# Kernel optimization log

Measured on AMD Instinct MI355X. Metric: run time of the kernel, lower is better.

Reference implementation:

```python
import jax, jax.numpy as jnp
import numpy as np

B, S, D, E, L = 8, 512, 768, 768, 4000

def setup_inputs() -> dict:
    key = jax.random.key(0)
    k1, k2, k3, k4 = jax.random.split(key, 4)
    last_hidden_state = jax.random.normal(k1, (B, S, D), dtype=jnp.float32)
    label_feat = jax.random.normal(k2, (L, E), dtype=jnp.float32)
    # nn.Linear(D, E): weight [E, D], bias [E]; xavier-ish scale
    W = jax.random.normal(k3, (E, D), dtype=jnp.float32) * (1.0 / np.sqrt(D))
    bias = jax.random.normal(k4, (E,), dtype=jnp.float32) * 0.01
    return {"last_hidden_state": last_hidden_state, "label_feat": label_feat, "W": W, "bias": bias}

def reference(last_hidden_state, label_feat, W, bias):
    # proj: tanh(Linear(last_hidden_state))  -> [B, S, E]
    proj = jnp.tanh(jnp.einsum('bsd,ed->bse', last_hidden_state, W) + bias)
    # scores: bmm(label_feat [B,L,E], proj^T [B,E,S]) -> [B, L, S]
    scores = jnp.einsum('le,bse->bls', label_feat, proj)
    # softmax over dim=1 (the LABEL dim), as in the original
    weights = jax.nn.softmax(scores, axis=1)
    # attn: bmm(weights [B,L,S], last_hidden_state [B,S,D]) -> [B, L, D]
    attn_output = jnp.einsum('bls,bsd->bld', weights, last_hidden_state)
    return (weights, attn_output)
```

## Files before the change

### kernel.cpp

```cpp
#include <hip/hip_runtime.h>
#include <hip/hip_bf16.h>
#include <cmath>

typedef __attribute__((ext_vector_type(8))) short short8;
typedef __attribute__((ext_vector_type(4))) float f32x4;

#define SM_CH 16
#define WCH   32

__device__ inline ushort f2bf(float x) {
    union { float f; unsigned u; } v; v.f = x;
    unsigned r = v.u + 0x7FFF + ((v.u >> 16) & 1);
    return (ushort)(r >> 16);
}

__device__ inline void split2(float x, ushort& hi, ushort& lo) {
    union { float f; unsigned u; } v; v.f = x;
    hi = (ushort)(v.u >> 16);
    union { float f; unsigned u; } h; h.u = v.u & 0xFFFF0000u;
    union { float f; unsigned u; } d; d.f = x - h.f;
    lo = (ushort)(d.u >> 16);
}

__device__ inline int swz(int row, int byte_in_row) {
    return row * 128 + (byte_in_row ^ ((row & 7) << 4));
}

__device__ inline void gload16(const void* g, void* lds) {
    __builtin_amdgcn_global_load_lds(
        (const __attribute__((address_space(1))) unsigned int*)g,
        (__attribute__((address_space(3))) unsigned int*)lds, 16, 0, 0);
}

__device__ inline void xcd_remap(int& bx, int& by, int& bz) {
    unsigned nx = gridDim.x, ny = gridDim.y;
    unsigned nwg = nx * ny * gridDim.z;
    unsigned id = blockIdx.x + nx * (blockIdx.y + ny * blockIdx.z);
    unsigned q = nwg >> 3;
    unsigned s = (id & 7) * q + (id >> 3);
    bx = s % nx; unsigned r = s / nx;
    by = r % ny; bz = r / ny;
}

__global__ __launch_bounds__(512, 2) void mfma_sc2(
    const ushort* __restrict__ AH, const ushort* __restrict__ AL,
    const ushort* __restrict__ BH, const ushort* __restrict__ BL,
    float* __restrict__ Cb, float* __restrict__ pmo, float* __restrict__ pso,
    int M, int N, long long sB, long long sC)
{
    extern __shared__ char smem[];
    const int K = 768;

    int bx, by, bz; xcd_remap(bx, by, bz);
    const int bm = bx * 256;
    const int bn = by * 256;
    const long long z = bz;

    const ushort* BHb = BH + z * sB;
    const ushort* BLb = BL + z * sB;

    const int t    = threadIdx.x;
    const int lane = t & 63;
    const int w    = t >> 6;
    const int wr   = w >> 2;
    const int wc   = w & 3;
    const int lrow = lane & 15;
    const int kg16 = (lane >> 4) * 16;

    const ushort* srcA[4]; const ushort* srcB[4]; int ldsO[4];
    #pragma unroll
    for (int i = 0; i < 4; ++i) {
        const int row  = w * 32 + i * 8 + (lane >> 3);
        const int q    = (lane & 7) ^ (row & 7);
        const int colo = (q & 3) * 8;
        srcA[i] = ((q < 4) ? AH : AL) + (long long)min(bm + row, M - 1) * K + colo;
        srcB[i] = ((q < 4) ? BHb : BLb) + (long long)(bn + row) * K + colo;
        ldsO[i] = w * 4096 + i * 1024;
    }

#define STAGE(k0_, cur_)                                                      \
    {                                                                         \
        _Pragma("unroll")                                                     \
        for (int i = 0; i < 4; ++i) {                                         \
            gload16(srcA[i] + (k0_), smem + (cur_) * 32768 + ldsO[i]);        \
            gload16(srcB[i] + (k0_), smem + 65536 + (cur_) * 32768 + ldsO[i]);\
        }                                                                     \
    }

    STAGE(0, 0);
    STAGE(32, 1);
    asm volatile("s_waitcnt vmcnt(8)" ::: "memory");
    __builtin_amdgcn_s_barrier();

    f32x4 acc[8][4] = {};

    for (int tt = 0; tt < 24; ++tt) {
        const int cur = tt & 1;
        const char* Ab = smem + cur * 32768;
        const char* Bb = smem + 65536 + cur * 32768;

        __builtin_amdgcn_s_setprio(1);
        short8 bh[4], bl[4];
        #pragma unroll
        for (int n = 0; n < 4; ++n) {
            bh[n] = *(const short8*)(Bb + swz(wc * 64 + n * 16 + lrow, kg16));
            bl[n] = *(const short8*)(Bb + swz(wc * 64 + n * 16 + lrow, 64 + kg16));
        }
        #pragma unroll
        for (int g = 0; g < 2; ++g) {
            short8 ah[4], al[4];
            #pragma unroll
            for (int m4 = 0; m4 < 4; ++m4) {
                const int r = wr * 128 + (g * 4 + m4) * 16 + lrow;
                ah[m4] = *(const short8*)(Ab + swz(r, kg16));
                al[m4] = *(const short8*)(Ab + swz(r, 64 + kg16));
            }
            #pragma unroll
            for (int m4 = 0; m4 < 4; ++m4)
                #pragma unroll
                for (int n = 0; n < 4; ++n) {
                    acc[g*4+m4][n] = __builtin_amdgcn_mfma_f32_16x16x32_bf16(
                        al[m4], bh[n], acc[g*4+m4][n], 0, 0, 0);
                    acc[g*4+m4][n] = __builtin_amdgcn_mfma_f32_16x16x32_bf16(
                        ah[m4], bl[n], acc[g*4+m4][n], 0, 0, 0);
                    acc[g*4+m4][n] = __builtin_amdgcn_mfma_f32_16x16x32_bf16(
                        ah[m4], bh[n], acc[g*4+m4][n], 0, 0, 0);
                }
        }
        __builtin_amdgcn_s_setprio(0);

        asm volatile("s_waitcnt lgkmcnt(0)" ::: "memory");
        __builtin_amdgcn_s_barrier();

        if (tt + 2 < 24) {
            STAGE((tt + 2) * 32, cur);
            asm volatile("s_waitcnt vmcnt(8)" ::: "memory");
        } else {
            asm volatile("s_waitcnt vmcnt(0)" ::: "memory");
        }
        __builtin_amdgcn_s_barrier();
    }
#undef STAGE

    float* C = Cb + z * sC;
    const int r0 = bm + wr * 128 + (lane >> 4) * 4;
    const int c0 = bn + wc * 64 + (lane & 15);
    #pragma unroll
    for (int n = 0; n < 4; ++n) {
        const int col = c0 + n * 16;
        #pragma unroll
        for (int mi = 0; mi < 8; ++mi) {
            #pragma unroll
            for (int r = 0; r < 4; ++r) {
                const int row = r0 + mi * 16 + r;
                if (row < M) C[(long long)row * N + col] = acc[mi][n][r];
            }
        }
    }

    __syncthreads();
    float* red = (float*)smem;
    const int slot = wr * 4 + (lane >> 4);
    const int colb = wc * 64 + (lane & 15);

    float lm[4];
    #pragma unroll
    for (int n = 0; n < 4; ++n) {
        float v = -INFINITY;
        #pragma unroll
        for (int mi = 0; mi < 8; ++mi)
            #pragma unroll
            for (int r = 0; r < 4; ++r)
                if (r0 + mi * 16 + r < M) v = fmaxf(v, acc[mi][n][r]);
        lm[n] = v;
    }
    #pragma unroll
    for (int n = 0; n < 4; ++n)
        red[(colb + n * 16) * 8 + slot] = lm[n];
    __syncthreads();
    float cm[4];
    #pragma unroll
    for (int n = 0; n < 4; ++n) {
        float v = -INFINITY;
        #pragma unroll
        for (int s8 = 0; s8 < 8; ++s8)
            v = fmaxf(v, red[(colb + n * 16) * 8 + s8]);
        cm[n] = v;
    }
    __syncthreads();
    float ls[4];
    #pragma unroll
    for (int n = 0; n < 4; ++n) {
        float sum = 0.f;
        #pragma unroll
        for (int mi = 0; mi < 8; ++mi)
            #pragma unroll
            for (int r = 0; r < 4; ++r)
                if (r0 + mi * 16 + r < M) sum += __expf(acc[mi][n][r] - cm[n]);
        ls[n] = sum;
    }
    #pragma unroll
    for (int n = 0; n < 4; ++n)
        red[(colb + n * 16) * 8 + slot] = ls[n];
    __syncthreads();
    if (slot == 0) {
        #pragma unroll
        for (int n = 0; n < 4; ++n) {
            float sum = 0.f;
            #pragma unroll
            for (int s8 = 0; s8 < 8; ++s8)
                sum += red[(colb + n * 16) * 8 + s8];
            const int col = bn + colb + n * 16;
            pmo[(z * SM_CH + bx) * N + col] = cm[n];
            pso[(z * SM_CH + bx) * N + col] = sum;
        }
    }
}

template<int ROWS, int KS>
__device__ inline void stage_plane(const ushort* __restrict__ src,
                                   char* plane, int t, int rbase, int rmax)
{
    #pragma unroll
    for (int s = 0; s < ROWS / 64; ++s) {
        const int row = s * 64 + (t >> 3);
        const int col = (((t & 7) * 16) ^ ((row & 7) << 4)) >> 1;
        const int gr  = min(rbase + row, rmax);
        gload16(src + (long long)gr * KS + col,
                plane + s * 8192 + (t >> 6) * 1024);
    }
}

__global__ __launch_bounds__(512, 2) void mfma_attn8(
    const ushort* __restrict__ A, const ushort* __restrict__ B,
    float* __restrict__ Cb, int M, int N,
    long long sA, long long sB, long long sC)
{
    extern __shared__ char smem[];
    constexpr int ABYTES = 128 * 128;
    constexpr int NT = 8, KS = 512;

    int bx, by, bz; xcd_remap(bx, by, bz);
    const int bm = bx * 128;
    const int bn = by * 256;
    const long long z = bz;

    const ushort* Ab_g = A + z * sA;
    const ushort* Bb_g = B + z * sB;

    const int t    = threadIdx.x;
    const int lane = t & 63;
    const int w    = t >> 6;
    const int wr   = w >> 2;
    const int wc   = w & 3;
    const int lrow = lane & 15;
    const int kg16 = (lane >> 4) * 16;

    stage_plane<128, KS>(Ab_g, smem, t, bm, M - 1);
    stage_plane<256, KS>(Bb_g, smem + 2 * ABYTES, t, bn, N - 1);
    stage_plane<128, KS>(Ab_g + 64, smem + ABYTES, t, bm, M - 1);
    stage_plane<256, KS>(Bb_g + 64, smem + 2 * ABYTES + 32768, t, bn, N - 1);
    asm volatile("s_waitcnt vmcnt(6)" ::: "memory");
    __builtin_amdgcn_s_barrier();

    f32x4 acc[4][4] = {};

    for (int tt = 0; tt < NT; ++tt) {
        const int cur = tt & 1;
        char* Ab = smem + cur * ABYTES;
        char* Bb = smem + 2 * ABYTES + cur * 32768;

        __builtin_amdgcn_s_setprio(1);
        short8 bf[4][2];
        #pragma unroll
        for (int n = 0; n < 4; ++n)
            #pragma unroll
            for (int ks = 0; ks < 2; ++ks)
                bf[n][ks] = *(const short8*)(Bb + swz(wc * 64 + n * 16 + lrow,
                                                      ks * 64 + kg16));
        #pragma unroll
        for (int q = 0; q < 2; ++q) {
            short8 af[2][2];
            #pragma unroll
            for (int mi = 0; mi < 2; ++mi)
                #pragma unroll
                for (int ks = 0; ks < 2; ++ks)
                    af[mi][ks] = *(const short8*)(Ab +
                        swz(wr * 64 + (q * 2 + mi) * 16 + lrow, ks * 64 + kg16));
            #pragma unroll
            for (int ks = 0; ks < 2; ++ks)
                #pragma unroll
                for (int mi = 0; mi < 2; ++mi)
                    #pragma unroll
                    for (int n = 0; n < 4; ++n)
                        acc[q * 2 + mi][n] = __builtin_amdgcn_mfma_f32_16x16x32_bf16(
                            af[mi][ks], bf[n][ks], acc[q * 2 + mi][n], 0, 0, 0);
        }
        __builtin_amdgcn_s_setprio(0);

        asm volatile("s_waitcnt lgkmcnt(0)" ::: "memory");
        __builtin_amdgcn_s_barrier();

        if (tt + 2 < NT) {
            stage_plane<128, KS>(Ab_g + (tt + 2) * 64, smem + cur * ABYTES,
                                 t, bm, M - 1);
            stage_plane<256, KS>(Bb_g + (tt + 2) * 64,
                                 smem + 2 * ABYTES + cur * 32768, t, bn, N - 1);
            asm volatile("s_waitcnt vmcnt(6)" ::: "memory");
        } else {
            asm volatile("s_waitcnt vmcnt(0)" ::: "memory");
        }
        __builtin_amdgcn_s_barrier();
    }

    float* C = Cb + z * sC;
    const int r0 = bm + wr * 64 + (lane >> 4) * 4;
    const int c0 = bn + wc * 64 + (lane & 15);
    #pragma unroll
    for (int n = 0; n < 4; ++n) {
        const int col = c0 + n * 16;
        #pragma unroll
        for (int mi = 0; mi < 4; ++mi) {
            #pragma unroll
            for (int r = 0; r < 4; ++r) {
                const int row = r0 + mi * 16 + r;
                if (row < M) C[(long long)row * N + col] = acc[mi][n][r];
            }
        }
    }
}

__global__ __launch_bounds__(256) void split_planes_kernel(
    const float* __restrict__ in, ushort* __restrict__ H,
    ushort* __restrict__ L, long long n4)
{
    long long i = (long long)blockIdx.x * 256 + threadIdx.x;
    if (i >= n4) return;
    float4 v = *(const float4*)(in + i * 4);
    ushort h[4], l[4];
    split2(v.x, h[0], l[0]); split2(v.y, h[1], l[1]);
    split2(v.z, h[2], l[2]); split2(v.w, h[3], l[3]);
    *(ushort4*)(H + i * 4) = *(ushort4*)h;
    *(ushort4*)(L + i * 4) = *(ushort4*)l;
}

__global__ __launch_bounds__(256) void mfma_proj2(
    const float* __restrict__ Ab, const ushort* __restrict__ WH,
    const ushort* __restrict__ WL, ushort* __restrict__ CH,
    ushort* __restrict__ CL, const float* __restrict__ bias,
    int M, int N, int K)
{
    extern __shared__ char smem[];
    char* Ah = smem;
    char* Al = smem + 16384;
    char* Bh = smem + 32768;
    char* Bl = smem + 49152;

    int bx, by, bz; xcd_remap(bx, by, bz);
    const int bm = bx * 128;
    const int bn = by * 128;

    const int t    = threadIdx.x;
    const int lane = t & 63;
    const int w    = t >> 6;

    const int srow = t >> 1;
    const int skh  = (t & 1) * 32;
    const float* ap = Ab + (long long)min(bm + srow, M - 1) * K + skh;

    const int lr  = lane >> 3;
    const int lc8 = 8 * ((lane & 7) ^ lr);
    const ushort* bh_src[4]; const ushort* bl_src[4];
    int ldsB[4];
    #pragma unroll
    for (int i = 0; i < 4; ++i) {
        const int row = w * 32 + i * 8 + lr;
        bh_src[i] = WH + (long long)(bn + row) * K + lc8;
        bl_src[i] = WL + (long long)(bn + row) * K + lc8;
        ldsB[i] = w * 4096 + i * 1024;
    }

    const int wm   = (w >> 1) * 64;
    const int wn   = (w & 1) * 64;
    const int lrow = lane & 15;
    const int kg16 = (lane >> 4) * 16;

    f32x4 acc[4][4] = {};

    for (int k0 = 0; k0 < K; k0 += 64) {
        #pragma unroll
        for (int i = 0; i < 4; ++i) {
            gload16(bh_src[i] + k0, Bh + ldsB[i]);
            gload16(bl_src[i] + k0, Bl + ldsB[i]);
        }
        #pragma unroll
        for (int j = 0; j < 4; ++j) {
            float xs[8];
            *(float4*)&xs[0] = *(const float4*)(ap + k0 + j * 8);
            *(float4*)&xs[4] = *(const float4*)(ap + k0 + j * 8 + 4);
            ushort oh[8], ol[8];
            #pragma unroll
            for (int i = 0; i < 8; ++i) split2(xs[i], oh[i], ol[i]);
            const int off = swz(srow, skh * 2 + j * 16);
            *(uint4*)(Ah + off) = *(uint4*)oh;
            *(uint4*)(Al + off) = *(uint4*)ol;
        }
        __syncthreads();

        #pragma unroll
        for (int kk = 0; kk < 2; ++kk) {
            short8 ah[4], al[4];
            #pragma unroll
            for (int mi = 0; mi < 4; ++mi) {
                const int off = swz(wm + mi * 16 + lrow, kk * 64 + kg16);
                ah[mi] = *(const short8*)(Ah + off);
                al[mi] = *(const short8*)(Al + off);
            }
            #pragma unroll
            for (int ni = 0; ni < 4; ++ni) {
                const int off = swz(wn + ni * 16 + lrow, kk * 64 + kg16);
                short8 bh = *(const short8*)(Bh + off);
                short8 bl = *(const short8*)(Bl + off);
                #pragma unroll
                for (int mi = 0; mi < 4; ++mi) {
                    acc[mi][ni] = __builtin_amdgcn_mfma_f32_16x16x32_bf16(al[mi], bh, acc[mi][ni], 0, 0, 0);
                    acc[mi][ni] = __builtin_amdgcn_mfma_f32_16x16x32_bf16(ah[mi], bl, acc[mi][ni], 0, 0, 0);
                    acc[mi][ni] = __builtin_amdgcn_mfma_f32_16x16x32_bf16(ah[mi], bh, acc[mi][ni], 0, 0, 0);
                }
            }
        }
        __syncthreads();
    }

    const int r0 = bm + wm + (lane >> 4) * 4;
    const int c0 = bn + wn + (lane & 15);
    #pragma unroll
    for (int ni = 0; ni < 4; ++ni) {
        const int col = c0 + ni * 16;
        const float bv = bias[col];
        #pragma unroll
        for (int mi = 0; mi < 4; ++mi) {
            #pragma unroll
            for (int r = 0; r < 4; ++r) {
                const int row = r0 + mi * 16 + r;
                if (row < M) {
                    float x = tanhf(acc[mi][ni][r] + bv);
                    ushort h, l;
                    split2(x, h, l);
                    CH[(long long)row * N + col] = h;
                    CL[(long long)row * N + col] = l;
                }
            }
        }
    }
}

__global__ __launch_bounds__(256) void transpose_bf16_kernel(
    const float* __restrict__ in, ushort* __restrict__ out, int S, int D)
{
    __shared__ float tile[32][33];
    const int b = blockIdx.z;
    const int s0 = blockIdx.x * 32, d0 = blockIdx.y * 32;
    const int tx = threadIdx.x & 31, ty = threadIdx.x >> 5;
    const float* ip = in + (long long)b * S * D;
    #pragma unroll
    for (int i = 0; i < 32; i += 8)
        tile[ty + i][tx] = ip[(long long)(s0 + ty + i) * D + d0 + tx];
    __syncthreads();
    ushort* op = out + (long long)b * S * D;
    #pragma unroll
    for (int i = 0; i < 32; i += 8)
        op[(long long)(d0 + ty + i) * S + s0 + tx] = f2bf(tile[tx][ty + i]);
}

__global__ __launch_bounds__(256) void softmax_write2_kernel(
    float* __restrict__ scores, const float* __restrict__ pm,
    const float* __restrict__ ps, int L, int S, int chlen,
    ushort* __restrict__ wbf)
{
    int s = blockIdx.x * 256 + threadIdx.x;
    int c = blockIdx.y;
    int b = blockIdx.z;

    float m = -INFINITY;
    #pragma unroll
    for (int k = 0; k < SM_CH; ++k)
        m = fmaxf(m, pm[(b * SM_CH + k) * S + s]);
    float sum = 0.f;
    #pragma unroll
    for (int k = 0; k < SM_CH; ++k)
        sum += ps[(b * SM_CH + k) * S + s] * __expf(pm[(b * SM_CH + k) * S + s] - m);
    float inv = 1.f / sum;

    float* p = scores + (long long)b * L * S + s;
    ushort* q = wbf + (long long)b * L * S + s;
    int l0 = c * chlen;
    int l1 = min(L, l0 + chlen);
    for (int l = l0; l < l1; ++l) {
        float x = p[(long long)l * S];
        float v = __expf(x - m) * inv;
        p[(long long)l * S] = v;
        q[(long long)l * S] = f2bf(v);
    }
}

extern "C" void kernel_launch(void* const* d_in, const int* in_sizes, int n_in,
                              void* d_out, int out_size, void* d_ws, size_t ws_size,
                              hipStream_t stream)
{
    const int Bn = 8, S = 512, D = 768, E = 768, L = 4000;
    const float* lhs   = (const float*)d_in[0];
    const float* label = (const float*)d_in[1];
    const float* W     = (const float*)d_in[2];
    const float* bias  = (const float*)d_in[3];

    float* weights = (float*)d_out;
    float* attn    = (float*)d_out + (long long)Bn * L * S;

    const long long nLE  = (long long)L * E;
    const long long nBSE = (long long)Bn * S * E;
    const long long nBDS = (long long)Bn * D * S;
    const long long nBLS = (long long)Bn * L * S;
    const long long nED  = (long long)E * D;

    ushort* labelH = (ushort*)d_ws;
    ushort* labelL = labelH + nLE;
    ushort* projH  = labelL + nLE;
    ushort* projL  = projH + nBSE;
    ushort* lhsT   = projL + nBSE;
    ushort* wbf    = lhsT + nBDS;
    float*  pm     = (float*)(wbf + nBLS);
    float*  ps     = pm + Bn * SM_CH * S;
    ushort* WH     = (ushort*)(ps + Bn * SM_CH * S);
    ushort* WL     = WH + nED;

    hipFuncSetAttribute((const void*)mfma_sc2,
                        hipFuncAttributeMaxDynamicSharedMemorySize, 131072);
    hipFuncSetAttribute((const void*)mfma_attn8,
                        hipFuncAttributeMaxDynamicSharedMemorySize, 98304);

    transpose_bf16_kernel<<<dim3(S / 32, D / 32, Bn), 256, 0, stream>>>(
        lhs, lhsT, S, D);
    split_planes_kernel<<<(int)(nLE / 4 + 255) / 256, 256, 0, stream>>>(
        label, labelH, labelL, nLE / 4);
    split_planes_kernel<<<(int)(nED / 4 + 255) / 256, 256, 0, stream>>>(
        W, WH, WL, nED / 4);

    mfma_proj2<<<dim3((Bn * S) / 128, E / 128, 1), 256, 65536, stream>>>(
        lhs, WH, WL, projH, projL, bias, Bn * S, E, D);

    mfma_sc2<<<dim3((L + 255) / 256, S / 256, Bn), 512, 131072, stream>>>(
        labelH, labelL, projH, projL, weights, pm, ps,
        L, S, (long long)S * E, (long long)L * S);

    softmax_write2_kernel<<<dim3(S / 256, WCH, Bn), 256, 0, stream>>>(
        weights, pm, ps, L, S, (L + WCH - 1) / WCH, wbf);

    mfma_attn8<<<dim3((L + 127) / 128, D / 256, Bn), 512, 98304, stream>>>(
        wbf, lhsT, attn, L, D,
        (long long)L * S, (long long)D * S, (long long)L * D);
}
```

Measured before the change: 238.7 us.

## Merge projection GEMM, input transpose and label split into one launch

Folds the transpose of the hidden state and the label-plane split into the projection GEMM kernel, with each role chosen by block index. The 192 GEMM blocks run first and the 3072 transpose blocks plus 3000 label-split blocks fill the otherwise idle CUs, removing two kernel launches and letting the independent prep work overlap the GEMM. The tradeoff is that every block now reserves 64KB of dynamic LDS even though the small branches need far less, which can limit occupancy for the elementwise blocks. Block indices and the GEMM tile mapping are hardcoded for these shapes.

```diff
diff --git a/kernel.cpp b/kernel.cpp
--- a/kernel.cpp
+++ b/kernel.cpp
@@ -344,133 +344,149 @@
     *(ushort4*)(L + i * 4) = *(ushort4*)l;
 }
 
-__global__ __launch_bounds__(256) void mfma_proj2(
-    const float* __restrict__ Ab, const ushort* __restrict__ WH,
+__global__ __launch_bounds__(256) void proj_prep_kernel(
+    const float* __restrict__ lhs, const ushort* __restrict__ WH,
     const ushort* __restrict__ WL, ushort* __restrict__ CH,
     ushort* __restrict__ CL, const float* __restrict__ bias,
-    int M, int N, int K)
+    ushort* __restrict__ lhsT, const float* __restrict__ label,
+    ushort* __restrict__ labelH, ushort* __restrict__ labelL,
+    int M, int N, int K, int S, int D, long long nLE4)
 {
     extern __shared__ char smem[];
-    char* Ah = smem;
-    char* Al = smem + 16384;
-    char* Bh = smem + 32768;
-    char* Bl = smem + 49152;
-
-    int bx, by, bz; xcd_remap(bx, by, bz);
-    const int bm = bx * 128;
-    const int bn = by * 128;
-
-    const int t    = threadIdx.x;
-    const int lane = t & 63;
-    const int w    = t >> 6;
-
-    const int srow = t >> 1;
-    const int skh  = (t & 1) * 32;
-    const float* ap = Ab + (long long)min(bm + srow, M - 1) * K + skh;
-
-    const int lr  = lane >> 3;
-    const int lc8 = 8 * ((lane & 7) ^ lr);
-    const ushort* bh_src[4]; const ushort* bl_src[4];
-    int ldsB[4];
-    #pragma unroll
-    for (int i = 0; i < 4; ++i) {
-        const int row = w * 32 + i * 8 + lr;
-        bh_src[i] = WH + (long long)(bn + row) * K + lc8;
-        bl_src[i] = WL + (long long)(bn + row) * K + lc8;
-        ldsB[i] = w * 4096 + i * 1024;
-    }
-
-    const int wm   = (w >> 1) * 64;
-    const int wn   = (w & 1) * 64;
-    const int lrow = lane & 15;
-    const int kg16 = (lane >> 4) * 16;
-
-    f32x4 acc[4][4] = {};
-
-    for (int k0 = 0; k0 < K; k0 += 64) {
+    const int bid = blockIdx.x;
+
+    if (bid < 192) {
+        char* Ah = smem;
+        char* Al = smem + 16384;
+        char* Bh = smem + 32768;
+        char* Bl = smem + 49152;
+
+        const unsigned sswz = (bid & 7) * 24 + (bid >> 3);
+        const int bx = sswz % 32, by = sswz / 32;
+        const int bm = bx * 128;
+        const int bn = by * 128;
+
+        const int t    = threadIdx.x;
+        const int lane = t & 63;
+        const int w    = t >> 6;
+
+        const int srow = t >> 1;
+        const int skh  = (t & 1) * 32;
+        const float* ap = lhs + (long long)min(bm + srow, M - 1) * K + skh;
+
+        const int lr  = lane >> 3;
+        const int lc8 = 8 * ((lane & 7) ^ lr);
+        const ushort* bh_src[4]; const ushort* bl_src[4];
+        int ldsB[4];
         #pragma unroll
         for (int i = 0; i < 4; ++i) {
-            gload16(bh_src[i] + k0, Bh + ldsB[i]);
-            gload16(bl_src[i] + k0, Bl + ldsB[i]);
-        }
-        #pragma unroll
-        for (int j = 0; j < 4; ++j) {
-            float xs[8];
-            *(float4*)&xs[0] = *(const float4*)(ap + k0 + j * 8);
-            *(float4*)&xs[4] = *(const float4*)(ap + k0 + j * 8 + 4);
-            ushort oh[8], ol[8];
-            #pragma unroll
-            for (int i = 0; i < 8; ++i) split2(xs[i], oh[i], ol[i]);
-            const int off = swz(srow, skh * 2 + j * 16);
-            *(uint4*)(Ah + off) = *(uint4*)oh;
-            *(uint4*)(Al + off) = *(uint4*)ol;
-        }
+            const int row = w * 32 + i * 8 + lr;
+            bh_src[i] = WH + (long long)(bn + row) * K + lc8;
+            bl_src[i] = WL + (long long)(bn + row) * K + lc8;
+            ldsB[i] = w * 4096 + i * 1024;
+        }
+
+        const int wm   = (w >> 1) * 64;
+        const int wn   = (w & 1) * 64;
+        const int lrow = lane & 15;
+        const int kg16 = (lane >> 4) * 16;
+
+        f32x4 acc[4][4] = {};
+
+        for (int k0 = 0; k0 < K; k0 += 64) {
+            #pragma unroll
+            for (int i = 0; i < 4; ++i) {
+                gload16(bh_src[i] + k0, Bh + ldsB[i]);
+                gload16(bl_src[i] + k0, Bl + ldsB[i]);
+            }
+            #pragma unroll
+            for (int j = 0; j < 4; ++j) {
+                float xs[8];
+                *(float4*)&xs[0] = *(const float4*)(ap + k0 + j * 8);
+                *(float4*)&xs[4] = *(const float4*)(ap + k0 + j * 8 + 4);
+                ushort oh[8], ol[8];
+                #pragma unroll
+                for (int i = 0; i < 8; ++i) split2(xs[i], oh[i], ol[i]);
+                const int off = swz(srow, skh * 2 + j * 16);
+                *(uint4*)(Ah + off) = *(uint4*)oh;
+                *(uint4*)(Al + off) = *(uint4*)ol;
+            }
+            __syncthreads();
+
+            #pragma unroll
+            for (int kk = 0; kk < 2; ++kk) {
+                short8 ah[4], al[4];
+                #pragma unroll
+                for (int mi = 0; mi < 4; ++mi) {
+                    const int off = swz(wm + mi * 16 + lrow, kk * 64 + kg16);
+                    ah[mi] = *(const short8*)(Ah + off);
+                    al[mi] = *(const short8*)(Al + off);
+                }
+                #pragma unroll
+                for (int ni = 0; ni < 4; ++ni) {
+                    const int off = swz(wn + ni * 16 + lrow, kk * 64 + kg16);
+                    short8 bh = *(const short8*)(Bh + off);
+                    short8 bl = *(const short8*)(Bl + off);
+                    #pragma unroll
+                    for (int mi = 0; mi < 4; ++mi) {
+                        acc[mi][ni] = __builtin_amdgcn_mfma_f32_16x16x32_bf16(al[mi], bh, acc[mi][ni], 0, 0, 0);
+                        acc[mi][ni] = __builtin_amdgcn_mfma_f32_16x16x32_bf16(ah[mi], bl, acc[mi][ni], 0, 0, 0);
+                        acc[mi][ni] = __builtin_amdgcn_mfma_f32_16x16x32_bf16(ah[mi], bh, acc[mi][ni], 0, 0, 0);
+                    }
+                }
+            }
+            __syncthreads();
+        }
+
+        const int r0 = bm + wm + (lane >> 4) * 4;
+        const int c0 = bn + wn + (lane & 15);
+        #pragma unroll
+        for (int ni = 0; ni < 4; ++ni) {
+            const int col = c0 + ni * 16;
+            const float bv = bias[col];
+            #pragma unroll
+            for (int mi = 0; mi < 4; ++mi) {
+                #pragma unroll
+                for (int r = 0; r < 4; ++r) {
+                    const int row = r0 + mi * 16 + r;
+                    if (row < M) {
+                        float x = tanhf(acc[mi][ni][r] + bv);
+                        ushort h, l;
+                        split2(x, h, l);
+                        CH[(long long)row * N + col] = h;
+                        CL[(long long)row * N + col] = l;
+                    }
+                }
+            }
+        }
+    } else if (bid < 3264) {
+        float* tile = (float*)smem;
+        const int tid = bid - 192;
+        const int sx = tid & 15;
+        const int dy = (tid >> 4) % 24;
+        const int b  = tid / 384;
+        const int s0 = sx * 32, d0 = dy * 32;
+        const int tx = threadIdx.x & 31, ty = threadIdx.x >> 5;
+        const float* ip = lhs + (long long)b * S * D;
+        #pragma unroll
+        for (int i = 0; i < 32; i += 8)
+            tile[(ty + i) * 33 + tx] = ip[(long long)(s0 + ty + i) * D + d0 + tx];
         __syncthreads();
-
-        #pragma unroll
-        for (int kk = 0; kk < 2; ++kk) {
-            short8 ah[4], al[4];
-            #pragma unroll
-            for (int mi = 0; mi < 4; ++mi) {
-                const int off = swz(wm + mi * 16 + lrow, kk * 64 + kg16);
-                ah[mi] = *(const short8*)(Ah + off);
-                al[mi] = *(const short8*)(Al + off);
-            }
-            #pragma unroll
-            for (int ni = 0; ni < 4; ++ni) {
-                const int off = swz(wn + ni * 16 + lrow, kk * 64 + kg16);
-                short8 bh = *(const short8*)(Bh + off);
-                short8 bl = *(const short8*)(Bl + off);
-                #pragma unroll
-                for (int mi = 0; mi < 4; ++mi) {
-                    acc[mi][ni] = __builtin_amdgcn_mfma_f32_16x16x32_bf16(al[mi], bh, acc[mi][ni], 0, 0, 0);
-                    acc[mi][ni] = __builtin_amdgcn_mfma_f32_16x16x32_bf16(ah[mi], bl, acc[mi][ni], 0, 0, 0);
-                    acc[mi][ni] = __builtin_amdgcn_mfma_f32_16x16x32_bf16(ah[mi], bh, acc[mi][ni], 0, 0, 0);
-                }
-            }
-        }
-        __syncthreads();
-    }
-
-    const int r0 = bm + wm + (lane >> 4) * 4;
-    const int c0 = bn + wn + (lane & 15);
-    #pragma unroll
-    for (int ni = 0; ni < 4; ++ni) {
-        const int col = c0 + ni * 16;
-        const float bv = bias[col];
-        #pragma unroll
-        for (int mi = 0; mi < 4; ++mi) {
-            #pragma unroll
-            for (int r = 0; r < 4; ++r) {
-                const int row = r0 + mi * 16 + r;
-                if (row < M) {
-                    float x = tanhf(acc[mi][ni][r] + bv);
-                    ushort h, l;
-                    split2(x, h, l);
-                    CH[(long long)row * N + col] = h;
-                    CL[(long long)row * N + col] = l;
-                }
-            }
-        }
-    }
-}
-
-__global__ __launch_bounds__(256) void transpose_bf16_kernel(
-    const float* __restrict__ in, ushort* __restrict__ out, int S, int D)
-{
-    __shared__ float tile[32][33];
-    const int b = blockIdx.z;
-    const int s0 = blockIdx.x * 32, d0 = blockIdx.y * 32;
-    const int tx = threadIdx.x & 31, ty = threadIdx.x >> 5;
-    const float* ip = in + (long long)b * S * D;
-    #pragma unroll
-    for (int i = 0; i < 32; i += 8)
-        tile[ty + i][tx] = ip[(long long)(s0 + ty + i) * D + d0 + tx];
-    __syncthreads();
-    ushort* op = out + (long long)b * S * D;
-    #pragma unroll
-    for (int i = 0; i < 32; i += 8)
-        op[(long long)(d0 + ty + i) * S + s0 + tx] = f2bf(tile[tx][ty + i]);
+        ushort* op = lhsT + (long long)b * S * D;
+        #pragma unroll
+        for (int i = 0; i < 32; i += 8)
+            op[(long long)(d0 + ty + i) * S + s0 + tx] = f2bf(tile[tx * 33 + ty + i]);
+    } else {
+        long long i = (long long)(bid - 3264) * 256 + threadIdx.x;
+        if (i < nLE4) {
+            float4 v = *(const float4*)(label + i * 4);
+            ushort h[4], l[4];
+            split2(v.x, h[0], l[0]); split2(v.y, h[1], l[1]);
+            split2(v.z, h[2], l[2]); split2(v.w, h[3], l[3]);
+            *(ushort4*)(labelH + i * 4) = *(ushort4*)h;
+            *(ushort4*)(labelL + i * 4) = *(ushort4*)l;
+        }
+    }
 }
 
 __global__ __launch_bounds__(256) void softmax_write2_kernel(
@@ -538,16 +554,16 @@
                         hipFuncAttributeMaxDynamicSharedMemorySize, 131072);
     hipFuncSetAttribute((const void*)mfma_attn8,
                         hipFuncAttributeMaxDynamicSharedMemorySize, 98304);
-
-    transpose_bf16_kernel<<<dim3(S / 32, D / 32, Bn), 256, 0, stream>>>(
-        lhs, lhsT, S, D);
-    split_planes_kernel<<<(int)(nLE / 4 + 255) / 256, 256, 0, stream>>>(
-        label, labelH, labelL, nLE / 4);
+    hipFuncSetAttribute((const void*)proj_prep_kernel,
+                        hipFuncAttributeMaxDynamicSharedMemorySize, 65536);
+
     split_planes_kernel<<<(int)(nED / 4 + 255) / 256, 256, 0, stream>>>(
         W, WH, WL, nED / 4);
 
-    mfma_proj2<<<dim3((Bn * S) / 128, E / 128, 1), 256, 65536, stream>>>(
-        lhs, WH, WL, projH, projL, bias, Bn * S, E, D);
+    proj_prep_kernel<<<6264, 256, 65536, stream>>>(
+        lhs, WH, WL, projH, projL, bias,
+        lhsT, label, labelH, labelL,
+        Bn * S, E, D, S, D, nLE / 4);
 
     mfma_sc2<<<dim3((L + 255) / 256, S / 256, Bn), 512, 131072, stream>>>(
         labelH, labelL, projH, projL, weights, pm, ps,
```

New measurement: 232.9 us. 2.5% less time.
